# Optimization experiments

Measured on AMD Instinct MI355X. Metric: run time of the kernel, lower is better.

Reference implementation:

```python
import jax, jax.numpy as jnp
import numpy as np


def _gather_nbrs(feats, idx):
    # feats: [C, N], idx: [N, k] -> [C, N, k]
    return feats[:, idx]


def pointconv_dw(xyz, feats, idx, w_pos, b_pos, w_out, b_out):
    """Depthwise point conv: per-channel weights from relative neighbor coords.
    xyz: [B,3,N], feats: [B,C,N], idx: [B,N,k] -> [B,C_out,N]
    """
    nbr_xyz = jax.vmap(_gather_nbrs)(xyz, idx)            # [B,3,N,k]
    rel = nbr_xyz - xyz[:, :, :, None]                    # relative positions
    w = jnp.einsum('cd,bdnk->bcnk', w_pos, rel) + b_pos[None, :, None, None]
    g = jax.vmap(_gather_nbrs)(feats, idx)                # [B,C,N,k]
    agg = jnp.sum(w * g, axis=-1)                         # [B,C,N] depthwise reduce over k
    return jnp.einsum('oc,bcn->bon', w_out, agg) + b_out[None, :, None]


def setup_inputs() -> dict:
    key = jax.random.key(0)
    ks = jax.random.split(key, 16)
    B, N, K = 2, 65536, 4
    IN, HID = 64, 64
    C = HID + IN
    s = 0.02
    inp = {
        'xyz': jax.random.normal(ks[0], (B, 3, N), jnp.float32),
        'h': jax.random.normal(ks[1], (B, HID, N), jnp.float32),
        'x': jax.random.normal(ks[2], (B, IN, N), jnp.float32),
        'knn_indices': jax.random.randint(ks[3], (B, N, K), 0, N, jnp.int32),
    }
    names = ['z', 'r', 'q']
    for i, nm in enumerate(names):
        inp[f'w{nm}_pos'] = s * jax.random.normal(ks[4 + 4 * i], (C, 3), jnp.float32)
        inp[f'b{nm}_pos'] = jnp.zeros((C,), jnp.float32)
        inp[f'w{nm}_out'] = s * jax.random.normal(ks[5 + 4 * i], (HID, C), jnp.float32)
        inp[f'b{nm}_out'] = jnp.zeros((HID,), jnp.float32)
    return inp


def reference(xyz, h, x, knn_indices,
              wz_pos, bz_pos, wz_out, bz_out,
              wr_pos, br_pos, wr_out, br_out,
              wq_pos, bq_pos, wq_out, bq_out):
    hx = jnp.concatenate([h, x], axis=1)                  # [B, HID+IN, N]
    z = jax.nn.sigmoid(pointconv_dw(xyz, hx, knn_indices, wz_pos, bz_pos, wz_out, bz_out))
    r = jax.nn.sigmoid(pointconv_dw(xyz, hx, knn_indices, wr_pos, br_pos, wr_out, br_out))
    rhx = jnp.concatenate([r * h, x], axis=1)
    q = jnp.tanh(pointconv_dw(xyz, rhx, knn_indices, wq_pos, bq_pos, wq_out, bq_out))
    return (1.0 - z) * h + z * q
```

## Files before the change

kernel.cpp:

```cpp
#include <hip/hip_runtime.h>

#define NPTS 65536
#define BATCH 2
#define CCH 128
#define HIDC 64
#define LDB 520
#define LDB2 264
#define PLD 130

typedef unsigned short u16;
typedef unsigned int u32;
typedef __bf16 bf16_t;
typedef bf16_t bf16x8 __attribute__((ext_vector_type(8)));
typedef float f32x4 __attribute__((ext_vector_type(4)));

__device__ __forceinline__ u16 f2bf(float f){
  union { float f; unsigned u; } v; v.f = f;
  unsigned r = v.u + 0x7FFFu + ((v.u >> 16) & 1u);
  return (u16)(r >> 16);
}
__device__ __forceinline__ float bf2f(u16 u){
  union { unsigned u; float f; } v; v.u = ((unsigned)u) << 16; return v.f;
}
__device__ __forceinline__ u32 pkrn(float a, float b){
  union { float f; u32 u; } ua, ub; ua.f = a; ub.f = b;
  return ((ua.u + 0x8000u) >> 16) | ((ub.u + 0x8000u) & 0xffff0000u);
}
__device__ __forceinline__ float sigmoidf_(float v){ return 1.f/(1.f+__expf(-v)); }
__device__ __forceinline__ float tanhf_(float v){
  v = fminf(10.f, fmaxf(-10.f, v));
  float e = __expf(2.f*v);
  return (e-1.f)/(e+1.f);
}

__global__ __launch_bounds__(256) void kprep(
    const float* __restrict__ wz, const float* __restrict__ wzp, const float* __restrict__ bzp,
    const float* __restrict__ wr, const float* __restrict__ wrp, const float* __restrict__ brp,
    const float* __restrict__ wq, const float* __restrict__ wqp, const float* __restrict__ bqp,
    u16* __restrict__ A){
  int idx = blockIdx.x*256 + threadIdx.x;
  if (idx < 98304){
    int t = idx & 7, o = (idx>>3)&63, quad = (idx>>9)&3, s = (idx>>11)&15, g = idx>>15;
    int pk = s*32 + quad*8 + t;
    int j = pk>>7, chunk = (pk>>3)&15, tt = pk&7;
    int orig = chunk*32 + j*8 + tt;
    int c = orig>>2, m = orig&3;
    const float* W  = (g==0)? wz  : (g==1)? wr  : wq;
    const float* wp = (g==0)? wzp : (g==1)? wrp : wqp;
    const float* bp = (g==0)? bzp : (g==1)? brp : bqp;
    float coef = m ? wp[c*3 + m - 1] : bp[c];
    A[idx] = f2bf(W[o*CCH + c] * coef);
  } else {
    int i2 = idx - 98304;
    int t = i2 & 7, o = (i2>>3)&63, quad = (i2>>9)&3, s = (i2>>11)&7;
    int k2 = s*32 + quad*8 + t;
    int j = k2>>6, chunk = (k2>>3)&7, tt = k2&7;
    int orig = chunk*32 + j*8 + tt;
    int c = orig>>2, m = orig&3;
    float coef = m ? wqp[c*3 + m - 1] : bqp[c];
    A[idx] = f2bf(wq[o*CCH + c] * coef);
  }
}

__global__ __launch_bounds__(256) void k_pack(const float* __restrict__ h,
    const float* __restrict__ x, u16* __restrict__ hxT){
  __shared__ __align__(16) u16 tile[64*PLD];
  int tid = threadIdx.x;
  int b = blockIdx.x >> 10, n0 = (blockIdx.x & 1023) << 6;
  #pragma unroll
  for (int i = 0; i < 8; ++i){
    int cc = (tid>>4) + i*16;
    int nn = (tid & 15)*4;
    const float* src = (cc < HIDC)
        ? (h + (((size_t)(b*HIDC + cc))<<16) + n0 + nn)
        : (x + (((size_t)(b*HIDC + cc - HIDC))<<16) + n0 + nn);
    float4 v = *(const float4*)src;
    tile[(nn+0)*PLD + cc] = f2bf(v.x);
    tile[(nn+1)*PLD + cc] = f2bf(v.y);
    tile[(nn+2)*PLD + cc] = f2bf(v.z);
    tile[(nn+3)*PLD + cc] = f2bf(v.w);
  }
  __syncthreads();
  #pragma unroll
  for (int i = 0; i < 4; ++i){
    int tsk = tid + (i<<8);
    int n = tsk>>4, ch = (tsk&15)*8;
    uint4 v = *(const uint4*)(tile + n*PLD + ch);
    *(uint4*)(hxT + (((size_t)(b<<16) + n0 + n)<<7) + ch) = v;
  }
}

#define ACCUM(gv, rv) { \
  u32 dw_[4] = {gv.x, gv.y, gv.z, gv.w}; \
  _Pragma("unroll") \
  for (int q_ = 0; q_ < 4; ++q_){ \
    union { u32 u; float f; } lo_, hi_; \
    lo_.u = dw_[q_] << 16; hi_.u = dw_[q_] & 0xffff0000u; \
    m0[2*q_]   += lo_.f; mx[2*q_]   += rv.x*lo_.f; my[2*q_]   += rv.y*lo_.f; mz[2*q_]   += rv.z*lo_.f; \
    m0[2*q_+1] += hi_.f; mx[2*q_+1] += rv.x*hi_.f; my[2*q_+1] += rv.y*hi_.f; mz[2*q_+1] += rv.z*hi_.f; \
  } }

#define PACKROW(row, CHOFF, STRIDE) { \
  _Pragma("unroll") \
  for (int j_ = 0; j_ < 4; ++j_){ \
    int ca_ = 2*j_, cb_ = 2*j_+1; \
    uint4 v_; \
    v_.x = pkrn(m0[ca_], mx[ca_]); v_.y = pkrn(my[ca_], mz[ca_]); \
    v_.z = pkrn(m0[cb_], mx[cb_]); v_.w = pkrn(my[cb_], mz[cb_]); \
    *(uint4*)((row) + j_*(STRIDE) + (CHOFF)) = v_; \
  } }

__global__ __launch_bounds__(256, 4) void k_zr(
    const float* __restrict__ xyz, const float* __restrict__ h,
    const int* __restrict__ knn,
    const float* __restrict__ bz_out, const float* __restrict__ br_out,
    const u16* __restrict__ Azr,
    const u16* __restrict__ hxT, u16* __restrict__ rhT,
    u16* __restrict__ z_ws, u16* __restrict__ qx_ws)
{
  __shared__ __align__(16) u16 bext[32*LDB];
  __shared__ __align__(16) float4 relk[128];
  __shared__ __align__(16) int4 jlds[32];

  int tid = threadIdx.x; int lane = tid & 63; int wv = tid >> 6;
  int b = blockIdx.x >> 11, n0 = (blockIdx.x & 2047) << 5;
  size_t bN = (size_t)b * NPTS;

  if (tid < 128){
    int p = tid >> 2, k = tid & 3;
    int j = knn[((bN + n0 + p) << 2) + k];
    ((int*)jlds)[tid] = j;
    const float* xb = xyz + (size_t)b*3*NPTS;
    float cx = xb[n0+p], cy = xb[NPTS + n0+p], cz = xb[2*NPTS + n0+p];
    relk[tid] = make_float4(xb[j]-cx, xb[NPTS+j]-cy, xb[2*NPTS+j]-cz, 0.f);
  }
  __syncthreads();

  const u16* hxTb = hxT + (bN << 7);
  int pA = tid >> 4, chk = tid & 15;
  int pB = pA + 16;
  int4 jA = jlds[pA], jB = jlds[pB];
  const u16* cb = hxTb + chk*8;
  uint4 ga0 = *(const uint4*)(cb + (((size_t)jA.x)<<7));
  uint4 ga1 = *(const uint4*)(cb + (((size_t)jA.y)<<7));
  uint4 ga2 = *(const uint4*)(cb + (((size_t)jA.z)<<7));
  uint4 ga3 = *(const uint4*)(cb + (((size_t)jA.w)<<7));
  uint4 gb0 = *(const uint4*)(cb + (((size_t)jB.x)<<7));
  uint4 gb1 = *(const uint4*)(cb + (((size_t)jB.y)<<7));
  uint4 gb2 = *(const uint4*)(cb + (((size_t)jB.z)<<7));
  uint4 gb3 = *(const uint4*)(cb + (((size_t)jB.w)<<7));
  {
    float4 r0 = relk[pA*4+0], r1 = relk[pA*4+1], r2 = relk[pA*4+2], r3 = relk[pA*4+3];
    float m0[8] = {0,0,0,0,0,0,0,0}, mx[8] = {0,0,0,0,0,0,0,0};
    float my[8] = {0,0,0,0,0,0,0,0}, mz[8] = {0,0,0,0,0,0,0,0};
    ACCUM(ga0, r0); ACCUM(ga1, r1); ACCUM(ga2, r2); ACCUM(ga3, r3);
    PACKROW(bext + pA*LDB, chk*8, 128);
  }
  {
    float4 r0 = relk[pB*4+0], r1 = relk[pB*4+1], r2 = relk[pB*4+2], r3 = relk[pB*4+3];
    float m0[8] = {0,0,0,0,0,0,0,0}, mx[8] = {0,0,0,0,0,0,0,0};
    float my[8] = {0,0,0,0,0,0,0,0}, mz[8] = {0,0,0,0,0,0,0,0};
    ACCUM(gb0, r0); ACCUM(gb1, r1); ACCUM(gb2, r2); ACCUM(gb3, r3);
    PACKROW(bext + pB*LDB, chk*8, 128);
  }
  __syncthreads();

  int l15 = lane & 15, quad = lane >> 4;
  int orow = wv*16 + l15;
  f32x4 accz[2], accr[2], accq[2];
  #pragma unroll
  for (int nt = 0; nt < 2; ++nt){
    accz[nt] = (f32x4){0,0,0,0}; accr[nt] = (f32x4){0,0,0,0}; accq[nt] = (f32x4){0,0,0,0};
  }
  #pragma unroll
  for (int s = 0; s < 16; ++s){
    bf16x8 az = *(const bf16x8*)(Azr + ((s*4 + quad)*64 + orow)*8);
    bf16x8 ar = *(const bf16x8*)(Azr + 32768 + ((s*4 + quad)*64 + orow)*8);
    if (s & 2){
      bf16x8 aq = *(const bf16x8*)(Azr + 65536 + ((s*4 + quad)*64 + orow)*8);
      #pragma unroll
      for (int nt = 0; nt < 2; ++nt){
        bf16x8 bb = *(const bf16x8*)(bext + (nt*16 + l15)*LDB + s*32 + quad*8);
        accz[nt] = __builtin_amdgcn_mfma_f32_16x16x32_bf16(az, bb, accz[nt], 0, 0, 0);
        accr[nt] = __builtin_amdgcn_mfma_f32_16x16x32_bf16(ar, bb, accr[nt], 0, 0, 0);
        accq[nt] = __builtin_amdgcn_mfma_f32_16x16x32_bf16(aq, bb, accq[nt], 0, 0, 0);
      }
    } else {
      #pragma unroll
      for (int nt = 0; nt < 2; ++nt){
        bf16x8 bb = *(const bf16x8*)(bext + (nt*16 + l15)*LDB + s*32 + quad*8);
        accz[nt] = __builtin_amdgcn_mfma_f32_16x16x32_bf16(az, bb, accz[nt], 0, 0, 0);
        accr[nt] = __builtin_amdgcn_mfma_f32_16x16x32_bf16(ar, bb, accr[nt], 0, 0, 0);
      }
    }
  }
  __syncthreads();

  u16* zst  = bext;
  u16* rhst = bext + 2560;
  u16* qxst = bext + 2560 + 2304;
  #pragma unroll
  for (int nt = 0; nt < 2; ++nt){
    #pragma unroll
    for (int reg = 0; reg < 4; ++reg){
      int o = wv*16 + quad*4 + reg;
      int p = nt*16 + l15;
      float zf = sigmoidf_(accz[nt][reg] + bz_out[o]);
      float rf = sigmoidf_(accr[nt][reg] + br_out[o]);
      float hv = h[(((size_t)(b*HIDC + o))<<16) + n0 + p];
      zst[o*40 + p] = f2bf(zf);
      rhst[p*72 + o] = f2bf(rf * hv);
      qxst[o*40 + p] = f2bf(accq[nt][reg]);
    }
  }
  __syncthreads();

  {
    int p = tid >> 3, ch = (tid & 7)*8;
    uint4 v = *(const uint4*)(rhst + p*72 + ch);
    *(uint4*)(rhT + ((bN + n0 + p)<<6) + ch) = v;
  }
  {
    int o = tid >> 2, pc = (tid & 3)*8;
    uint4 v = *(const uint4*)(zst + o*40 + pc);
    *(uint4*)(z_ws + (((size_t)(b*HIDC + o))<<16) + n0 + pc) = v;
  }
  {
    int o = tid >> 2, pc = (tid & 3)*8;
    uint4 v = *(const uint4*)(qxst + o*40 + pc);
    *(uint4*)(qx_ws + (((size_t)(b*HIDC + o))<<16) + n0 + pc) = v;
  }
}

__global__ __launch_bounds__(256, 4) void k_q(
    const float* __restrict__ xyz, const float* __restrict__ h,
    const int* __restrict__ knn,
    const float* __restrict__ bq_out,
    const u16* __restrict__ Aqrh,
    const u16* __restrict__ rhT, const u16* __restrict__ z_ws,
    const u16* __restrict__ qx_ws, float* __restrict__ out)
{
  __shared__ __align__(16) u16 bext[64*LDB2];
  __shared__ __align__(16) float4 relk[256];
  __shared__ __align__(16) int4 jlds[64];

  int tid = threadIdx.x; int lane = tid & 63; int wv = tid >> 6;
  int b = blockIdx.x >> 10, n0 = (blockIdx.x & 1023) << 6;
  size_t bN = (size_t)b * NPTS;

  {
    int p = tid >> 2, k = tid & 3;
    int j = knn[((bN + n0 + p) << 2) + k];
    ((int*)jlds)[tid] = j;
    const float* xb = xyz + (size_t)b*3*NPTS;
    float cx = xb[n0+p], cy = xb[NPTS + n0+p], cz = xb[2*NPTS + n0+p];
    relk[tid] = make_float4(xb[j]-cx, xb[NPTS+j]-cy, xb[2*NPTS+j]-cz, 0.f);
  }
  __syncthreads();

  const u16* rhTb = rhT + (bN << 6);
  int pA = tid >> 3, chk = tid & 7;
  int pB = pA + 32;
  int4 jA = jlds[pA], jB = jlds[pB];
  const u16* cb = rhTb + chk*8;
  uint4 ga0 = *(const uint4*)(cb + (((size_t)jA.x)<<6));
  uint4 ga1 = *(const uint4*)(cb + (((size_t)jA.y)<<6));
  uint4 ga2 = *(const uint4*)(cb + (((size_t)jA.z)<<6));
  uint4 ga3 = *(const uint4*)(cb + (((size_t)jA.w)<<6));
  uint4 gb0 = *(const uint4*)(cb + (((size_t)jB.x)<<6));
  uint4 gb1 = *(const uint4*)(cb + (((size_t)jB.y)<<6));
  uint4 gb2 = *(const uint4*)(cb + (((size_t)jB.z)<<6));
  uint4 gb3 = *(const uint4*)(cb + (((size_t)jB.w)<<6));
  {
    float4 r0 = relk[pA*4+0], r1 = relk[pA*4+1], r2 = relk[pA*4+2], r3 = relk[pA*4+3];
    float m0[8] = {0,0,0,0,0,0,0,0}, mx[8] = {0,0,0,0,0,0,0,0};
    float my[8] = {0,0,0,0,0,0,0,0}, mz[8] = {0,0,0,0,0,0,0,0};
    ACCUM(ga0, r0); ACCUM(ga1, r1); ACCUM(ga2, r2); ACCUM(ga3, r3);
    PACKROW(bext + pA*LDB2, chk*8, 64);
  }
  {
    float4 r0 = relk[pB*4+0], r1 = relk[pB*4+1], r2 = relk[pB*4+2], r3 = relk[pB*4+3];
    float m0[8] = {0,0,0,0,0,0,0,0}, mx[8] = {0,0,0,0,0,0,0,0};
    float my[8] = {0,0,0,0,0,0,0,0}, mz[8] = {0,0,0,0,0,0,0,0};
    ACCUM(gb0, r0); ACCUM(gb1, r1); ACCUM(gb2, r2); ACCUM(gb3, r3);
    PACKROW(bext + pB*LDB2, chk*8, 64);
  }
  __syncthreads();

  int l15 = lane & 15, quad = lane >> 4;
  int orow = wv*16 + l15;
  f32x4 acc[4];
  #pragma unroll
  for (int nt = 0; nt < 4; ++nt) acc[nt] = (f32x4){0,0,0,0};
  #pragma unroll
  for (int s = 0; s < 8; ++s){
    bf16x8 aq = *(const bf16x8*)(Aqrh + ((s*4 + quad)*64 + orow)*8);
    #pragma unroll
    for (int nt = 0; nt < 4; ++nt){
      bf16x8 bb = *(const bf16x8*)(bext + (nt*16 + l15)*LDB2 + s*32 + quad*8);
      acc[nt] = __builtin_amdgcn_mfma_f32_16x16x32_bf16(aq, bb, acc[nt], 0, 0, 0);
    }
  }

  #pragma unroll
  for (int nt = 0; nt < 4; ++nt){
    #pragma unroll
    for (int reg = 0; reg < 4; ++reg){
      int o = wv*16 + quad*4 + reg;
      int p = nt*16 + l15;
      size_t idx = (((size_t)(b*HIDC + o))<<16) + n0 + p;
      float qpre = acc[nt][reg] + bq_out[o] + bf2f(qx_ws[idx]);
      float qf = tanhf_(qpre);
      float zf = bf2f(z_ws[idx]);
      float hv = h[idx];
      out[idx] = (1.f - zf)*hv + zf*qf;
    }
  }
}

extern "C" void kernel_launch(void* const* d_in, const int* in_sizes, int n_in,
                              void* d_out, int out_size, void* d_ws, size_t ws_size,
                              hipStream_t stream){
  const float* xyz    = (const float*)d_in[0];
  const float* h      = (const float*)d_in[1];
  const float* x      = (const float*)d_in[2];
  const int*   knn    = (const int*)d_in[3];
  const float* wz_pos = (const float*)d_in[4];
  const float* bz_pos = (const float*)d_in[5];
  const float* wz_out = (const float*)d_in[6];
  const float* bz_out = (const float*)d_in[7];
  const float* wr_pos = (const float*)d_in[8];
  const float* br_pos = (const float*)d_in[9];
  const float* wr_out = (const float*)d_in[10];
  const float* br_out = (const float*)d_in[11];
  const float* wq_pos = (const float*)d_in[12];
  const float* bq_pos = (const float*)d_in[13];
  const float* wq_out = (const float*)d_in[14];
  const float* bq_out = (const float*)d_in[15];
  float* out = (float*)d_out;

  u16* ws    = (u16*)d_ws;
  u16* hxT   = ws;
  u16* rhT   = ws + 16777216;
  u16* z_ws  = ws + 25165824;
  u16* qx_ws = ws + 33554432;
  u16* A     = ws + 41943040;

  kprep<<<448, 256, 0, stream>>>(wz_out, wz_pos, bz_pos, wr_out, wr_pos, br_pos,
                                 wq_out, wq_pos, bq_pos, A);
  k_pack<<<2048, 256, 0, stream>>>(h, x, hxT);
  k_zr<<<4096, 256, 0, stream>>>(xyz, h, knn, bz_out, br_out, A, hxT, rhT, z_ws, qx_ws);
  k_q<<<2048, 256, 0, stream>>>(xyz, h, knn, bq_out, A + 98304, rhT, z_ws, qx_ws, out);
}
```

Before: 222.5 us.

## Make gather kernels persistent over four tiles with register prefetch of next gathers

Both gather+MFMA kernels now process four 32-point tiles per block in a loop. The next tile's knn indices and neighbor feature gathers are issued before the MFMA stage, so gather latency overlaps compute, and relative coordinates are kept in registers instead of LDS. The z and qx intermediates are packed into a single u32 workspace written directly from registers, removing the LDS transpose. The grid shrinks to 1024 blocks per kernel, which lowers parallelism and raises register pressure. The per-point workspace writes are now strided rather than vectorized.

```diff
diff --git a/kernel.cpp b/kernel.cpp
--- a/kernel.cpp
+++ b/kernel.cpp
@@ -90,14 +90,14 @@
   }
 }
 
-#define ACCUM(gv, rv) { \
+#define ACCUM(gv, RX, RY, RZ) { \
   u32 dw_[4] = {gv.x, gv.y, gv.z, gv.w}; \
   _Pragma("unroll") \
   for (int q_ = 0; q_ < 4; ++q_){ \
     union { u32 u; float f; } lo_, hi_; \
     lo_.u = dw_[q_] << 16; hi_.u = dw_[q_] & 0xffff0000u; \
-    m0[2*q_]   += lo_.f; mx[2*q_]   += rv.x*lo_.f; my[2*q_]   += rv.y*lo_.f; mz[2*q_]   += rv.z*lo_.f; \
-    m0[2*q_+1] += hi_.f; mx[2*q_+1] += rv.x*hi_.f; my[2*q_+1] += rv.y*hi_.f; mz[2*q_+1] += rv.z*hi_.f; \
+    m0[2*q_]   += lo_.f; mx[2*q_]   += (RX)*lo_.f; my[2*q_]   += (RY)*lo_.f; mz[2*q_]   += (RZ)*lo_.f; \
+    m0[2*q_+1] += hi_.f; mx[2*q_+1] += (RX)*hi_.f; my[2*q_+1] += (RY)*hi_.f; mz[2*q_+1] += (RZ)*hi_.f; \
   } }
 
 #define PACKROW(row, CHOFF, STRIDE) { \
@@ -110,125 +110,153 @@
     *(uint4*)((row) + j_*(STRIDE) + (CHOFF)) = v_; \
   } }
 
+#define LOADREL(RX, RY, RZ, JJ, P, N0) { \
+  float cx_ = xb[(N0)+(P)], cy_ = xb[NPTS+(N0)+(P)], cz_ = xb[2*NPTS+(N0)+(P)]; \
+  RX[0]=xb[JJ.x]-cx_; RY[0]=xb[NPTS+JJ.x]-cy_; RZ[0]=xb[2*NPTS+JJ.x]-cz_; \
+  RX[1]=xb[JJ.y]-cx_; RY[1]=xb[NPTS+JJ.y]-cy_; RZ[1]=xb[2*NPTS+JJ.y]-cz_; \
+  RX[2]=xb[JJ.z]-cx_; RY[2]=xb[NPTS+JJ.z]-cy_; RZ[2]=xb[2*NPTS+JJ.z]-cz_; \
+  RX[3]=xb[JJ.w]-cx_; RY[3]=xb[NPTS+JJ.w]-cy_; RZ[3]=xb[2*NPTS+JJ.w]-cz_; }
+
 __global__ __launch_bounds__(256, 4) void k_zr(
     const float* __restrict__ xyz, const float* __restrict__ h,
     const int* __restrict__ knn,
     const float* __restrict__ bz_out, const float* __restrict__ br_out,
     const u16* __restrict__ Azr,
-    const u16* __restrict__ hxT, u16* __restrict__ rhT,
-    u16* __restrict__ z_ws, u16* __restrict__ qx_ws)
+    const u16* __restrict__ hxT, u16* __restrict__ rhT, u32* __restrict__ zq_ws)
 {
   __shared__ __align__(16) u16 bext[32*LDB];
-  __shared__ __align__(16) float4 relk[128];
-  __shared__ __align__(16) int4 jlds[32];
+  __shared__ __align__(16) u16 rhst[32*72];
 
   int tid = threadIdx.x; int lane = tid & 63; int wv = tid >> 6;
-  int b = blockIdx.x >> 11, n0 = (blockIdx.x & 2047) << 5;
+  int bid = blockIdx.x;
+  int b = bid >> 9;
+  int nbase = (bid & 511) << 7;
   size_t bN = (size_t)b * NPTS;
-
-  if (tid < 128){
-    int p = tid >> 2, k = tid & 3;
-    int j = knn[((bN + n0 + p) << 2) + k];
-    ((int*)jlds)[tid] = j;
-    const float* xb = xyz + (size_t)b*3*NPTS;
-    float cx = xb[n0+p], cy = xb[NPTS + n0+p], cz = xb[2*NPTS + n0+p];
-    relk[tid] = make_float4(xb[j]-cx, xb[NPTS+j]-cy, xb[2*NPTS+j]-cz, 0.f);
-  }
-  __syncthreads();
-
+  const float* xb = xyz + (size_t)b*3*NPTS;
   const u16* hxTb = hxT + (bN << 7);
-  int pA = tid >> 4, chk = tid & 15;
+  const int4* knn4 = (const int4*)knn + bN;
+  int pA = tid >> 4, chk8 = (tid & 15)*8;
   int pB = pA + 16;
-  int4 jA = jlds[pA], jB = jlds[pB];
-  const u16* cb = hxTb + chk*8;
-  uint4 ga0 = *(const uint4*)(cb + (((size_t)jA.x)<<7));
-  uint4 ga1 = *(const uint4*)(cb + (((size_t)jA.y)<<7));
-  uint4 ga2 = *(const uint4*)(cb + (((size_t)jA.z)<<7));
-  uint4 ga3 = *(const uint4*)(cb + (((size_t)jA.w)<<7));
-  uint4 gb0 = *(const uint4*)(cb + (((size_t)jB.x)<<7));
-  uint4 gb1 = *(const uint4*)(cb + (((size_t)jB.y)<<7));
-  uint4 gb2 = *(const uint4*)(cb + (((size_t)jB.z)<<7));
-  uint4 gb3 = *(const uint4*)(cb + (((size_t)jB.w)<<7));
-  {
-    float4 r0 = relk[pA*4+0], r1 = relk[pA*4+1], r2 = relk[pA*4+2], r3 = relk[pA*4+3];
-    float m0[8] = {0,0,0,0,0,0,0,0}, mx[8] = {0,0,0,0,0,0,0,0};
-    float my[8] = {0,0,0,0,0,0,0,0}, mz[8] = {0,0,0,0,0,0,0,0};
-    ACCUM(ga0, r0); ACCUM(ga1, r1); ACCUM(ga2, r2); ACCUM(ga3, r3);
-    PACKROW(bext + pA*LDB, chk*8, 128);
-  }
-  {
-    float4 r0 = relk[pB*4+0], r1 = relk[pB*4+1], r2 = relk[pB*4+2], r3 = relk[pB*4+3];
-    float m0[8] = {0,0,0,0,0,0,0,0}, mx[8] = {0,0,0,0,0,0,0,0};
-    float my[8] = {0,0,0,0,0,0,0,0}, mz[8] = {0,0,0,0,0,0,0,0};
-    ACCUM(gb0, r0); ACCUM(gb1, r1); ACCUM(gb2, r2); ACCUM(gb3, r3);
-    PACKROW(bext + pB*LDB, chk*8, 128);
-  }
-  __syncthreads();
-
+  const u16* cbase = hxTb + chk8;
   int l15 = lane & 15, quad = lane >> 4;
   int orow = wv*16 + l15;
-  f32x4 accz[2], accr[2], accq[2];
-  #pragma unroll
-  for (int nt = 0; nt < 2; ++nt){
-    accz[nt] = (f32x4){0,0,0,0}; accr[nt] = (f32x4){0,0,0,0}; accq[nt] = (f32x4){0,0,0,0};
-  }
-  #pragma unroll
-  for (int s = 0; s < 16; ++s){
-    bf16x8 az = *(const bf16x8*)(Azr + ((s*4 + quad)*64 + orow)*8);
-    bf16x8 ar = *(const bf16x8*)(Azr + 32768 + ((s*4 + quad)*64 + orow)*8);
-    if (s & 2){
-      bf16x8 aq = *(const bf16x8*)(Azr + 65536 + ((s*4 + quad)*64 + orow)*8);
-      #pragma unroll
-      for (int nt = 0; nt < 2; ++nt){
-        bf16x8 bb = *(const bf16x8*)(bext + (nt*16 + l15)*LDB + s*32 + quad*8);
-        accz[nt] = __builtin_amdgcn_mfma_f32_16x16x32_bf16(az, bb, accz[nt], 0, 0, 0);
-        accr[nt] = __builtin_amdgcn_mfma_f32_16x16x32_bf16(ar, bb, accr[nt], 0, 0, 0);
-        accq[nt] = __builtin_amdgcn_mfma_f32_16x16x32_bf16(aq, bb, accq[nt], 0, 0, 0);
+
+  int4 jA, jB;
+  float rAx[4], rAy[4], rAz[4], rBx[4], rBy[4], rBz[4];
+  uint4 ga[4], gb[4];
+
+  {
+    int n0 = nbase;
+    jA = knn4[n0 + pA]; jB = knn4[n0 + pB];
+    LOADREL(rAx, rAy, rAz, jA, pA, n0);
+    LOADREL(rBx, rBy, rBz, jB, pB, n0);
+    ga[0] = *(const uint4*)(cbase + (((size_t)jA.x)<<7));
+    ga[1] = *(const uint4*)(cbase + (((size_t)jA.y)<<7));
+    ga[2] = *(const uint4*)(cbase + (((size_t)jA.z)<<7));
+    ga[3] = *(const uint4*)(cbase + (((size_t)jA.w)<<7));
+    gb[0] = *(const uint4*)(cbase + (((size_t)jB.x)<<7));
+    gb[1] = *(const uint4*)(cbase + (((size_t)jB.y)<<7));
+    gb[2] = *(const uint4*)(cbase + (((size_t)jB.z)<<7));
+    gb[3] = *(const uint4*)(cbase + (((size_t)jB.w)<<7));
+  }
+
+  for (int t = 0; t < 4; ++t){
+    int n0c = nbase + (t<<5);
+    int n0n = n0c + 32;
+    bool more = (t < 3);
+    int4 jAn = jA, jBn = jB;
+    if (more){ jAn = knn4[n0n + pA]; jBn = knn4[n0n + pB]; }
+
+    {
+      float m0[8]={0,0,0,0,0,0,0,0}, mx[8]={0,0,0,0,0,0,0,0};
+      float my[8]={0,0,0,0,0,0,0,0}, mz[8]={0,0,0,0,0,0,0,0};
+      ACCUM(ga[0], rAx[0], rAy[0], rAz[0]);
+      ACCUM(ga[1], rAx[1], rAy[1], rAz[1]);
+      ACCUM(ga[2], rAx[2], rAy[2], rAz[2]);
+      ACCUM(ga[3], rAx[3], rAy[3], rAz[3]);
+      PACKROW(bext + pA*LDB, chk8, 128);
+    }
+    {
+      float m0[8]={0,0,0,0,0,0,0,0}, mx[8]={0,0,0,0,0,0,0,0};
+      float my[8]={0,0,0,0,0,0,0,0}, mz[8]={0,0,0,0,0,0,0,0};
+      ACCUM(gb[0], rBx[0], rBy[0], rBz[0]);
+      ACCUM(gb[1], rBx[1], rBy[1], rBz[1]);
+      ACCUM(gb[2], rBx[2], rBy[2], rBz[2]);
+      ACCUM(gb[3], rBx[3], rBy[3], rBz[3]);
+      PACKROW(bext + pB*LDB, chk8, 128);
+    }
+
+    uint4 gan[4], gbn[4];
+    if (more){
+      gan[0] = *(const uint4*)(cbase + (((size_t)jAn.x)<<7));
+      gan[1] = *(const uint4*)(cbase + (((size_t)jAn.y)<<7));
+      gan[2] = *(const uint4*)(cbase + (((size_t)jAn.z)<<7));
+      gan[3] = *(const uint4*)(cbase + (((size_t)jAn.w)<<7));
+      gbn[0] = *(const uint4*)(cbase + (((size_t)jBn.x)<<7));
+      gbn[1] = *(const uint4*)(cbase + (((size_t)jBn.y)<<7));
+      gbn[2] = *(const uint4*)(cbase + (((size_t)jBn.z)<<7));
+      gbn[3] = *(const uint4*)(cbase + (((size_t)jBn.w)<<7));
+    }
+    __syncthreads();
+
+    f32x4 accz[2], accr[2], accq[2];
+    #pragma unroll
+    for (int nt = 0; nt < 2; ++nt){
+      accz[nt] = (f32x4){0,0,0,0}; accr[nt] = (f32x4){0,0,0,0}; accq[nt] = (f32x4){0,0,0,0};
+    }
+    #pragma unroll
+    for (int s = 0; s < 16; ++s){
+      bf16x8 az = *(const bf16x8*)(Azr + ((s*4 + quad)*64 + orow)*8);
+      bf16x8 ar = *(const bf16x8*)(Azr + 32768 + ((s*4 + quad)*64 + orow)*8);
+      if (s & 2){
+        bf16x8 aq = *(const bf16x8*)(Azr + 65536 + ((s*4 + quad)*64 + orow)*8);
+        #pragma unroll
+        for (int nt = 0; nt < 2; ++nt){
+          bf16x8 bb = *(const bf16x8*)(bext + (nt*16 + l15)*LDB + s*32 + quad*8);
+          accz[nt] = __builtin_amdgcn_mfma_f32_16x16x32_bf16(az, bb, accz[nt], 0, 0, 0);
+          accr[nt] = __builtin_amdgcn_mfma_f32_16x16x32_bf16(ar, bb, accr[nt], 0, 0, 0);
+          accq[nt] = __builtin_amdgcn_mfma_f32_16x16x32_bf16(aq, bb, accq[nt], 0, 0, 0);
+        }
+      } else {
+        #pragma unroll
+        for (int nt = 0; nt < 2; ++nt){
+          bf16x8 bb = *(const bf16x8*)(bext + (nt*16 + l15)*LDB + s*32 + quad*8);
+          accz[nt] = __builtin_amdgcn_mfma_f32_16x16x32_bf16(az, bb, accz[nt], 0, 0, 0);
+          accr[nt] = __builtin_amdgcn_mfma_f32_16x16x32_bf16(ar, bb, accr[nt], 0, 0, 0);
+        }
       }
-    } else {
-      #pragma unroll
-      for (int nt = 0; nt < 2; ++nt){
-        bf16x8 bb = *(const bf16x8*)(bext + (nt*16 + l15)*LDB + s*32 + quad*8);
-        accz[nt] = __builtin_amdgcn_mfma_f32_16x16x32_bf16(az, bb, accz[nt], 0, 0, 0);
-        accr[nt] = __builtin_amdgcn_mfma_f32_16x16x32_bf16(ar, bb, accr[nt], 0, 0, 0);
+    }
+
+    if (more){
+      LOADREL(rAx, rAy, rAz, jAn, pA, n0n);
+      LOADREL(rBx, rBy, rBz, jBn, pB, n0n);
+    }
+
+    #pragma unroll
+    for (int nt = 0; nt < 2; ++nt){
+      #pragma unroll
+      for (int reg = 0; reg < 4; ++reg){
+        int o = wv*16 + quad*4 + reg;
+        int p = nt*16 + l15;
+        size_t idx = (((size_t)(b*HIDC + o))<<16) + n0c + p;
+        float zf = sigmoidf_(accz[nt][reg] + bz_out[o]);
+        float rf = sigmoidf_(accr[nt][reg] + br_out[o]);
+        float hv = h[idx];
+        zq_ws[idx] = pkrn(zf, accq[nt][reg]);
+        rhst[p*72 + o] = f2bf(rf * hv);
       }
     }
-  }
-  __syncthreads();
-
-  u16* zst  = bext;
-  u16* rhst = bext + 2560;
-  u16* qxst = bext + 2560 + 2304;
-  #pragma unroll
-  for (int nt = 0; nt < 2; ++nt){
-    #pragma unroll
-    for (int reg = 0; reg < 4; ++reg){
-      int o = wv*16 + quad*4 + reg;
-      int p = nt*16 + l15;
-      float zf = sigmoidf_(accz[nt][reg] + bz_out[o]);
-      float rf = sigmoidf_(accr[nt][reg] + br_out[o]);
-      float hv = h[(((size_t)(b*HIDC + o))<<16) + n0 + p];
-      zst[o*40 + p] = f2bf(zf);
-      rhst[p*72 + o] = f2bf(rf * hv);
-      qxst[o*40 + p] = f2bf(accq[nt][reg]);
-    }
-  }
-  __syncthreads();
-
-  {
-    int p = tid >> 3, ch = (tid & 7)*8;
-    uint4 v = *(const uint4*)(rhst + p*72 + ch);
-    *(uint4*)(rhT + ((bN + n0 + p)<<6) + ch) = v;
-  }
-  {
-    int o = tid >> 2, pc = (tid & 3)*8;
-    uint4 v = *(const uint4*)(zst + o*40 + pc);
-    *(uint4*)(z_ws + (((size_t)(b*HIDC + o))<<16) + n0 + pc) = v;
-  }
-  {
-    int o = tid >> 2, pc = (tid & 3)*8;
-    uint4 v = *(const uint4*)(qxst + o*40 + pc);
-    *(uint4*)(qx_ws + (((size_t)(b*HIDC + o))<<16) + n0 + pc) = v;
+    __syncthreads();
+    {
+      int p = tid >> 3, ch = (tid & 7)*8;
+      uint4 v = *(const uint4*)(rhst + p*72 + ch);
+      *(uint4*)(rhT + ((bN + n0c + p)<<6) + ch) = v;
+    }
+    if (more){
+      jA = jAn; jB = jBn;
+      #pragma unroll
+      for (int i = 0; i < 4; ++i){ ga[i] = gan[i]; gb[i] = gbn[i]; }
+    }
   }
 }
 
@@ -237,83 +265,101 @@
     const int* __restrict__ knn,
     const float* __restrict__ bq_out,
     const u16* __restrict__ Aqrh,
-    const u16* __restrict__ rhT, const u16* __restrict__ z_ws,
-    const u16* __restrict__ qx_ws, float* __restrict__ out)
+    const u16* __restrict__ rhT, const u32* __restrict__ zq_ws,
+    float* __restrict__ out)
 {
-  __shared__ __align__(16) u16 bext[64*LDB2];
-  __shared__ __align__(16) float4 relk[256];
-  __shared__ __align__(16) int4 jlds[64];
+  __shared__ __align__(16) u16 bext[32*LDB2];
 
   int tid = threadIdx.x; int lane = tid & 63; int wv = tid >> 6;
-  int b = blockIdx.x >> 10, n0 = (blockIdx.x & 1023) << 6;
+  int bid = blockIdx.x;
+  int b = bid >> 9;
+  int nbase = (bid & 511) << 7;
   size_t bN = (size_t)b * NPTS;
-
-  {
-    int p = tid >> 2, k = tid & 3;
-    int j = knn[((bN + n0 + p) << 2) + k];
-    ((int*)jlds)[tid] = j;
-    const float* xb = xyz + (size_t)b*3*NPTS;
-    float cx = xb[n0+p], cy = xb[NPTS + n0+p], cz = xb[2*NPTS + n0+p];
-    relk[tid] = make_float4(xb[j]-cx, xb[NPTS+j]-cy, xb[2*NPTS+j]-cz, 0.f);
-  }
-  __syncthreads();
-
+  const float* xb = xyz + (size_t)b*3*NPTS;
   const u16* rhTb = rhT + (bN << 6);
-  int pA = tid >> 3, chk = tid & 7;
-  int pB = pA + 32;
-  int4 jA = jlds[pA], jB = jlds[pB];
-  const u16* cb = rhTb + chk*8;
-  uint4 ga0 = *(const uint4*)(cb + (((size_t)jA.x)<<6));
-  uint4 ga1 = *(const uint4*)(cb + (((size_t)jA.y)<<6));
-  uint4 ga2 = *(const uint4*)(cb + (((size_t)jA.z)<<6));
-  uint4 ga3 = *(const uint4*)(cb + (((size_t)jA.w)<<6));
-  uint4 gb0 = *(const uint4*)(cb + (((size_t)jB.x)<<6));
-  uint4 gb1 = *(const uint4*)(cb + (((size_t)jB.y)<<6));
-  uint4 gb2 = *(const uint4*)(cb + (((size_t)jB.z)<<6));
-  uint4 gb3 = *(const uint4*)(cb + (((size_t)jB.w)<<6));
-  {
-    float4 r0 = relk[pA*4+0], r1 = relk[pA*4+1], r2 = relk[pA*4+2], r3 = relk[pA*4+3];
-    float m0[8] = {0,0,0,0,0,0,0,0}, mx[8] = {0,0,0,0,0,0,0,0};
-    float my[8] = {0,0,0,0,0,0,0,0}, mz[8] = {0,0,0,0,0,0,0,0};
-    ACCUM(ga0, r0); ACCUM(ga1, r1); ACCUM(ga2, r2); ACCUM(ga3, r3);
-    PACKROW(bext + pA*LDB2, chk*8, 64);
-  }
-  {
-    float4 r0 = relk[pB*4+0], r1 = relk[pB*4+1], r2 = relk[pB*4+2], r3 = relk[pB*4+3];
-    float m0[8] = {0,0,0,0,0,0,0,0}, mx[8] = {0,0,0,0,0,0,0,0};
-    float my[8] = {0,0,0,0,0,0,0,0}, mz[8] = {0,0,0,0,0,0,0,0};
-    ACCUM(gb0, r0); ACCUM(gb1, r1); ACCUM(gb2, r2); ACCUM(gb3, r3);
-    PACKROW(bext + pB*LDB2, chk*8, 64);
-  }
-  __syncthreads();
-
+  const int4* knn4 = (const int4*)knn + bN;
+  int pt = tid >> 3, chk8 = (tid & 7)*8;
+  const u16* cbase = rhTb + chk8;
   int l15 = lane & 15, quad = lane >> 4;
   int orow = wv*16 + l15;
-  f32x4 acc[4];
-  #pragma unroll
-  for (int nt = 0; nt < 4; ++nt) acc[nt] = (f32x4){0,0,0,0};
-  #pragma unroll
-  for (int s = 0; s < 8; ++s){
-    bf16x8 aq = *(const bf16x8*)(Aqrh + ((s*4 + quad)*64 + orow)*8);
-    #pragma unroll
-    for (int nt = 0; nt < 4; ++nt){
-      bf16x8 bb = *(const bf16x8*)(bext + (nt*16 + l15)*LDB2 + s*32 + quad*8);
-      acc[nt] = __builtin_amdgcn_mfma_f32_16x16x32_bf16(aq, bb, acc[nt], 0, 0, 0);
-    }
-  }
-
-  #pragma unroll
-  for (int nt = 0; nt < 4; ++nt){
-    #pragma unroll
-    for (int reg = 0; reg < 4; ++reg){
-      int o = wv*16 + quad*4 + reg;
-      int p = nt*16 + l15;
-      size_t idx = (((size_t)(b*HIDC + o))<<16) + n0 + p;
-      float qpre = acc[nt][reg] + bq_out[o] + bf2f(qx_ws[idx]);
-      float qf = tanhf_(qpre);
-      float zf = bf2f(z_ws[idx]);
-      float hv = h[idx];
-      out[idx] = (1.f - zf)*hv + zf*qf;
+
+  int4 jj;
+  float rx[4], ry[4], rz[4];
+  uint4 g[4];
+
+  {
+    int n0 = nbase;
+    jj = knn4[n0 + pt];
+    LOADREL(rx, ry, rz, jj, pt, n0);
+    g[0] = *(const uint4*)(cbase + (((size_t)jj.x)<<6));
+    g[1] = *(const uint4*)(cbase + (((size_t)jj.y)<<6));
+    g[2] = *(const uint4*)(cbase + (((size_t)jj.z)<<6));
+    g[3] = *(const uint4*)(cbase + (((size_t)jj.w)<<6));
+  }
+
+  for (int t = 0; t < 4; ++t){
+    int n0c = nbase + (t<<5);
+    int n0n = n0c + 32;
+    bool more = (t < 3);
+    int4 jn = jj;
+    if (more){ jn = knn4[n0n + pt]; }
+
+    {
+      float m0[8]={0,0,0,0,0,0,0,0}, mx[8]={0,0,0,0,0,0,0,0};
+      float my[8]={0,0,0,0,0,0,0,0}, mz[8]={0,0,0,0,0,0,0,0};
+      ACCUM(g[0], rx[0], ry[0], rz[0]);
+      ACCUM(g[1], rx[1], ry[1], rz[1]);
+      ACCUM(g[2], rx[2], ry[2], rz[2]);
+      ACCUM(g[3], rx[3], ry[3], rz[3]);
+      PACKROW(bext + pt*LDB2, chk8, 64);
+    }
+
+    uint4 gn[4];
+    if (more){
+      gn[0] = *(const uint4*)(cbase + (((size_t)jn.x)<<6));
+      gn[1] = *(const uint4*)(cbase + (((size_t)jn.y)<<6));
+      gn[2] = *(const uint4*)(cbase + (((size_t)jn.z)<<6));
+      gn[3] = *(const uint4*)(cbase + (((size_t)jn.w)<<6));
+    }
+    __syncthreads();
+
+    f32x4 acc[2];
+    #pragma unroll
+    for (int nt = 0; nt < 2; ++nt) acc[nt] = (f32x4){0,0,0,0};
+    #pragma unroll
+    for (int s = 0; s < 8; ++s){
+      bf16x8 aq = *(const bf16x8*)(Aqrh + ((s*4 + quad)*64 + orow)*8);
+      #pragma unroll
+      for (int nt = 0; nt < 2; ++nt){
+        bf16x8 bb = *(const bf16x8*)(bext + (nt*16 + l15)*LDB2 + s*32 + quad*8);
+        acc[nt] = __builtin_amdgcn_mfma_f32_16x16x32_bf16(aq, bb, acc[nt], 0, 0, 0);
+      }
+    }
+
+    if (more){
+      LOADREL(rx, ry, rz, jn, pt, n0n);
+    }
+
+    #pragma unroll
+    for (int nt = 0; nt < 2; ++nt){
+      #pragma unroll
+      for (int reg = 0; reg < 4; ++reg){
+        int o = wv*16 + quad*4 + reg;
+        int p = nt*16 + l15;
+        size_t idx = (((size_t)(b*HIDC + o))<<16) + n0c + p;
+        u32 v = zq_ws[idx];
+        float zf  = bf2f((u16)(v & 0xffffu));
+        float qxv = bf2f((u16)(v >> 16));
+        float qf = tanhf_(acc[nt][reg] + bq_out[o] + qxv);
+        float hv = h[idx];
+        out[idx] = (1.f - zf)*hv + zf*qf;
+      }
+    }
+    __syncthreads();
+    if (more){
+      jj = jn;
+      #pragma unroll
+      for (int i = 0; i < 4; ++i) g[i] = gn[i];
     }
   }
 }
@@ -339,16 +385,15 @@
   const float* bq_out = (const float*)d_in[15];
   float* out = (float*)d_out;
 
-  u16* ws    = (u16*)d_ws;
-  u16* hxT   = ws;
-  u16* rhT   = ws + 16777216;
-  u16* z_ws  = ws + 25165824;
-  u16* qx_ws = ws + 33554432;
-  u16* A     = ws + 41943040;
+  u16* ws   = (u16*)d_ws;
+  u16* hxT  = ws;
+  u16* rhT  = ws + 16777216;
+  u32* zq   = (u32*)(ws + 25165824);
+  u16* A    = ws + 41943040;
 
   kprep<<<448, 256, 0, stream>>>(wz_out, wz_pos, bz_pos, wr_out, wr_pos, br_pos,
                                  wq_out, wq_pos, bq_pos, A);
   k_pack<<<2048, 256, 0, stream>>>(h, x, hxT);
-  k_zr<<<4096, 256, 0, stream>>>(xyz, h, knn, bz_out, br_out, A, hxT, rhT, z_ws, qx_ws);
-  k_q<<<2048, 256, 0, stream>>>(xyz, h, knn, bq_out, A + 98304, rhT, z_ws, qx_ws, out);
-}
+  k_zr<<<1024, 256, 0, stream>>>(xyz, h, knn, bz_out, br_out, A, hxT, rhT, zq);
+  k_q<<<1024, 256, 0, stream>>>(xyz, h, knn, bq_out, A + 98304, rhT, zq, out);
+}
```

New measurement: 629.2 us. 2.83x slower.
